# Kernel optimization log

Measured on AMD Instinct MI355X. Metric: run time of the kernel, lower is better.

## Reference

```python
import jax, jax.numpy as jnp
import numpy as np

N_H = 2048
N_EXC = 1638  # Dale's law: first N_EXC neurons excitatory, rest inhibitory
TAU_E, TAU_I = 0.02, 0.01
DT = 0.001
U_MIN_E, U_MAX_E = -5.0, 5.0
U_MIN_I, U_MAX_I = -5.0, 5.0
B, TR, T = 16, 4, 256


def setup_inputs() -> dict:
    key = jax.random.key(0)
    k1, k2, k3, k4, k5 = jax.random.split(key, 5)
    u0 = jax.random.normal(k1, (B, TR, N_H), dtype=jnp.float32)
    fs = jax.random.normal(k2, (B, TR, T, N_H), dtype=jnp.float32)
    # noise[..., 0, :] = eta0; noise[..., t, :] = eta used at step t; noise[..., T, :] = final eta
    noise = jax.random.normal(k3, (B, TR, T + 1, N_H), dtype=jnp.float32) * 0.1
    W_rec = jax.random.normal(k4, (N_H, N_H), dtype=jnp.float32) / np.sqrt(N_H)
    bias = jax.random.normal(k5, (N_H,), dtype=jnp.float32) * 0.01
    return {"u0": u0, "fs": fs, "noise": noise, "W_rec": W_rec, "bias": bias}


def _const_vectors():
    is_exc = jnp.arange(N_H) < N_EXC
    tau_inv = jnp.where(is_exc, 1.0 / TAU_E, 1.0 / TAU_I).astype(jnp.float32)  # diag(tau_inv) as vector
    u_max = jnp.where(is_exc, U_MAX_E, U_MAX_I).astype(jnp.float32)
    u_min = jnp.where(is_exc, U_MIN_E, U_MIN_I).astype(jnp.float32)
    return tau_inv, u_min, u_max


def reference(u0, fs, noise, W_rec, bias):
    tau_inv, u_min, u_max = _const_vectors()

    def step(u, inp):
        f, eta = inp  # each [B, TR, N_H]
        r = jax.nn.relu(u)  # rate_activation
        rec = jnp.einsum('btn,mn->btm', r, W_rec)  # W_rec(r), Linear-style r @ W^T
        du_dt = (-u + f + rec + bias + eta) * tau_inv  # @ diag(tau_inv)
        u_new = jnp.clip(u + du_dt * DT, u_min, u_max)
        return u_new, (u_new, du_dt)

    fs_t = jnp.moveaxis(fs, 2, 0)              # [T, B, TR, N_H]
    eta_t = jnp.moveaxis(noise[:, :, :T], 2, 0)  # [T, B, TR, N_H]
    _, (u_hist, du_hist) = jax.lax.scan(step, u0, (fs_t, eta_t))
    u_history = jnp.moveaxis(u_hist, 0, 2)     # [B, TR, T, N_H]
    du_dt_history = jnp.moveaxis(du_hist, 0, 2)
    eta_final = noise[:, :, T]
    return u_history, eta_final, du_dt_history
```

## Files before the change

### kernel.cpp

```cpp
#include <hip/hip_runtime.h>


#define N_H     2048
#define N_EXC   1638
#define T_STEPS 256
#define BT_TOT  64

typedef __bf16 bf16_t;
typedef __attribute__((ext_vector_type(8))) __bf16 bf16x8;
typedef __attribute__((ext_vector_type(4))) float  f32x4;
typedef __attribute__((ext_vector_type(2))) float  f32x2;

__global__ __launch_bounds__(256, 1)
void rnn_persistent(const float* __restrict__ u0,
                    const float* __restrict__ fs,
                    const float* __restrict__ noise,
                    const float* __restrict__ Wrec,
                    const float* __restrict__ bias,
                    float* __restrict__ out,
                    bf16_t* __restrict__ rbuf,
                    int* __restrict__ flags)
{
    const int g    = blockIdx.x;
    const int bti  = g >> 6;
    const int mi   = g & 63;
    const int tid  = threadIdx.x;
    const int wave = tid >> 6;
    const int lane = tid & 63;
    const int l15  = lane & 15;
    const int quad = lane >> 4;

    const int bt0 = bti * 16;
    const int m0  = mi * 32;
    const int kw0 = wave * 512;

    float* u_hist  = out;
    float* eta_out = out + (size_t)BT_TOT * T_STEPS * N_H;
    float* du_hist = eta_out + (size_t)BT_TOT * N_H;

    const int row  = tid >> 4;
    const int bt   = bt0 + row;
    const int nloc = (tid & 15) * 2;
    const int n0   = m0 + nloc;
    const int tile = nloc >> 4;
    const int col  = nloc & 15;
    const int srcl = (row >> 2) * 16 + col;
    const int reg  = row & 3;

    const f32x2 bv  = *(const f32x2*)(bias + n0);
    const float ti0 = (n0     < N_EXC) ? 50.0f : 100.0f;
    const float ti1 = (n0 + 1 < N_EXC) ? 50.0f : 100.0f;

    f32x2 uv = *(const f32x2*)(u0 + (size_t)bt * N_H + n0);
    float uA = uv.x, uB = uv.y;

    {
      union { bf16_t h[2]; unsigned int w; } rp;
      rp.h[0] = (bf16_t)fmaxf(uA, 0.0f);
      rp.h[1] = (bf16_t)fmaxf(uB, 0.0f);
      __hip_atomic_store((unsigned int*)(rbuf + (size_t)bt * N_H + n0), rp.w,
                         __ATOMIC_RELAXED, __HIP_MEMORY_SCOPE_AGENT);
    }
    asm volatile("s_waitcnt vmcnt(0)" ::: "memory");
    __syncthreads();
    if (tid == 0)
      __hip_atomic_store(&flags[g], 1, __ATOMIC_RELAXED, __HIP_MEMORY_SCOPE_AGENT);

    bf16x8 Wf[16][2];
#pragma unroll
    for (int kk = 0; kk < 16; ++kk) {
#pragma unroll
      for (int tl = 0; tl < 2; ++tl) {
        const float* wp = Wrec + (size_t)(m0 + tl*16 + l15) * N_H
                               + (kw0 + kk*32 + quad*8);
        f32x4 w0 = *(const f32x4*)(wp);
        f32x4 w1 = *(const f32x4*)(wp + 4);
        bf16x8 v;
#pragma unroll
        for (int j = 0; j < 4; ++j) { v[j] = (bf16_t)w0[j]; v[4+j] = (bf16_t)w1[j]; }
        Wf[kk][tl] = v;
      }
    }

    __shared__ float red[4][2][64][4];

    const size_t half = (size_t)BT_TOT * N_H;

    for (int t = 0; t < T_STEPS; ++t) {
      f32x2 fv = *(const f32x2*)(fs    + ((size_t)bt * T_STEPS       + t) * N_H + n0);
      f32x2 ev = *(const f32x2*)(noise + ((size_t)bt * (T_STEPS + 1) + t) * N_H + n0);

      if (wave == 0) {
        const int fi = (bti << 6) | lane;
        int cnt = 0;
        for (;;) {
          int v = __hip_atomic_load(&flags[fi], __ATOMIC_RELAXED,
                                    __HIP_MEMORY_SCOPE_AGENT);
          if (__all(v >= t + 1)) break;
          if (++cnt > (1 << 18)) break;
          __builtin_amdgcn_s_sleep(2);
        }
      }
      __syncthreads();

      const bf16_t* rsrc  = rbuf + (size_t)(t & 1) * half;
      const bf16_t* abase = rsrc + (size_t)(bt0 + l15) * N_H + (kw0 + quad * 8);
      bf16x8 af[16];
#define LOADA(I, OFFS) \
      asm volatile("global_load_dwordx4 %0, %1, off offset:" OFFS " sc0 sc1" \
                   : "=v"(af[I]) : "v"(abase) : "memory")
      LOADA(0,"0");    LOADA(1,"64");   LOADA(2,"128");  LOADA(3,"192");
      LOADA(4,"256");  LOADA(5,"320");  LOADA(6,"384");  LOADA(7,"448");
      LOADA(8,"512");  LOADA(9,"576");  LOADA(10,"640"); LOADA(11,"704");
      LOADA(12,"768"); LOADA(13,"832"); LOADA(14,"896"); LOADA(15,"960");
#undef LOADA
      asm volatile("s_waitcnt vmcnt(0)" ::: "memory");
      __builtin_amdgcn_sched_barrier(0);

      f32x4 acc0 = {0.f,0.f,0.f,0.f}, acc1 = {0.f,0.f,0.f,0.f};
#pragma unroll
      for (int kk = 0; kk < 16; ++kk) {
        acc0 = __builtin_amdgcn_mfma_f32_16x16x32_bf16(af[kk], Wf[kk][0], acc0, 0, 0, 0);
        acc1 = __builtin_amdgcn_mfma_f32_16x16x32_bf16(af[kk], Wf[kk][1], acc1, 0, 0, 0);
      }

      *reinterpret_cast<f32x4*>(&red[wave][0][lane][0]) = acc0;
      *reinterpret_cast<f32x4*>(&red[wave][1][lane][0]) = acc1;
      __syncthreads();

      float rec0 = red[0][tile][srcl][reg]     + red[1][tile][srcl][reg]
                 + red[2][tile][srcl][reg]     + red[3][tile][srcl][reg];
      float rec1 = red[0][tile][srcl + 1][reg] + red[1][tile][srcl + 1][reg]
                 + red[2][tile][srcl + 1][reg] + red[3][tile][srcl + 1][reg];

      float du0 = (-uA + fv.x + rec0 + bv.x + ev.x) * ti0;
      float du1 = (-uB + fv.y + rec1 + bv.y + ev.y) * ti1;
      float un0 = fminf(fmaxf(uA + du0 * 0.001f, -5.0f), 5.0f);
      float un1 = fminf(fmaxf(uB + du1 * 0.001f, -5.0f), 5.0f);
      uA = un0; uB = un1;

      {
        bf16_t* rdst = rbuf + (size_t)((t + 1) & 1) * half;
        union { bf16_t h[2]; unsigned int w; } rp;
        rp.h[0] = (bf16_t)fmaxf(un0, 0.0f);
        rp.h[1] = (bf16_t)fmaxf(un1, 0.0f);
        __hip_atomic_store((unsigned int*)(rdst + (size_t)bt * N_H + n0), rp.w,
                           __ATOMIC_RELAXED, __HIP_MEMORY_SCOPE_AGENT);
      }

      asm volatile("s_waitcnt vmcnt(0)" ::: "memory");
      __syncthreads();
      if (tid == 0)
        __hip_atomic_store(&flags[g], t + 2, __ATOMIC_RELAXED,
                           __HIP_MEMORY_SCOPE_AGENT);

      const size_t o = ((size_t)bt * T_STEPS + t) * N_H + n0;
      f32x2 uo; uo.x = un0; uo.y = un1;
      f32x2 dd; dd.x = du0; dd.y = du1;
      *(f32x2*)(u_hist + o)  = uo;
      *(f32x2*)(du_hist + o) = dd;
    }

    f32x2 ef = *(const f32x2*)(noise + ((size_t)bt * (T_STEPS + 1) + T_STEPS) * N_H + n0);
    *(f32x2*)(eta_out + (size_t)bt * N_H + n0) = ef;
}

extern "C" void kernel_launch(void* const* d_in, const int* in_sizes, int n_in,
                              void* d_out, int out_size, void* d_ws, size_t ws_size,
                              hipStream_t stream) {
    const float* u0    = (const float*)d_in[0];
    const float* fs    = (const float*)d_in[1];
    const float* noise = (const float*)d_in[2];
    const float* Wrec  = (const float*)d_in[3];
    const float* bias  = (const float*)d_in[4];
    float* out = (float*)d_out;

    int*    flags = (int*)d_ws;
    bf16_t* rbuf  = (bf16_t*)((char*)d_ws + 4096);

    hipMemsetAsync(d_ws, 0, 4096, stream);

    rnn_persistent<<<dim3(256), dim3(256), 0, stream>>>(
        u0, fs, noise, Wrec, bias, out, rbuf, flags);
}
```

Before: 1.789 ms.

## Use per-wave flags, drop block barriers, and pipeline MFMA with partial waitcnt

Replaces the per-block flag and block-wide barriers around the grid-wide step handshake with per-wave flags, so each wave signals and polls its own flags independently. All four waves now spin on the flags, burning FMAs instead of s_sleep. The reduction LDS buffer is double-buffered by step parity so the block barrier after the store can be removed. MFMA issue is split into four groups, each gated by a partial vmcnt wait so compute can overlap the remaining A-fragment loads. The risks are more polling traffic on the flags (four times as many, with four waves spinning) and subtle ordering issues from the removed barriers, and the flag array grows to 1024 ints.

Result: no change. 1.820 ms (+1.7%).

```diff
diff --git a/kernel.cpp b/kernel.cpp
--- a/kernel.cpp
+++ b/kernel.cpp
@@ -62,9 +62,9 @@
                          __ATOMIC_RELAXED, __HIP_MEMORY_SCOPE_AGENT);
     }
     asm volatile("s_waitcnt vmcnt(0)" ::: "memory");
-    __syncthreads();
-    if (tid == 0)
-      __hip_atomic_store(&flags[g], 1, __ATOMIC_RELAXED, __HIP_MEMORY_SCOPE_AGENT);
+    if (lane == 0)
+      __hip_atomic_store(&flags[(g << 2) | wave], 1,
+                         __ATOMIC_RELAXED, __HIP_MEMORY_SCOPE_AGENT);
 
     bf16x8 Wf[16][2];
 #pragma unroll
@@ -82,26 +82,31 @@
       }
     }
 
-    __shared__ float red[4][2][64][4];
+    __shared__ float red[2][4][2][65][4];
 
     const size_t half = (size_t)BT_TOT * N_H;
+    const int fi = (bti << 8) | (wave << 6) | lane;
 
     for (int t = 0; t < T_STEPS; ++t) {
       f32x2 fv = *(const f32x2*)(fs    + ((size_t)bt * T_STEPS       + t) * N_H + n0);
       f32x2 ev = *(const f32x2*)(noise + ((size_t)bt * (T_STEPS + 1) + t) * N_H + n0);
 
-      if (wave == 0) {
-        const int fi = (bti << 6) | lane;
+      {
+        float z0 = 1.0f + (float)lane * 1e-7f, z1 = 2.0f;
         int cnt = 0;
         for (;;) {
           int v = __hip_atomic_load(&flags[fi], __ATOMIC_RELAXED,
                                     __HIP_MEMORY_SCOPE_AGENT);
           if (__all(v >= t + 1)) break;
-          if (++cnt > (1 << 18)) break;
-          __builtin_amdgcn_s_sleep(2);
+          if (++cnt > (1 << 17)) break;
+#pragma unroll
+          for (int s = 0; s < 8; ++s) {
+            z0 = __builtin_fmaf(z0, 1.0000001f, 1e-20f);
+            z1 = __builtin_fmaf(z1, 0.9999999f, 1e-20f);
+          }
         }
+        asm volatile("" :: "v"(z0), "v"(z1));
       }
-      __syncthreads();
 
       const bf16_t* rsrc  = rbuf + (size_t)(t & 1) * half;
       const bf16_t* abase = rsrc + (size_t)(bt0 + l15) * N_H + (kw0 + quad * 8);
@@ -114,24 +119,34 @@
       LOADA(8,"512");  LOADA(9,"576");  LOADA(10,"640"); LOADA(11,"704");
       LOADA(12,"768"); LOADA(13,"832"); LOADA(14,"896"); LOADA(15,"960");
 #undef LOADA
-      asm volatile("s_waitcnt vmcnt(0)" ::: "memory");
-      __builtin_amdgcn_sched_barrier(0);
 
       f32x4 acc0 = {0.f,0.f,0.f,0.f}, acc1 = {0.f,0.f,0.f,0.f};
-#pragma unroll
-      for (int kk = 0; kk < 16; ++kk) {
-        acc0 = __builtin_amdgcn_mfma_f32_16x16x32_bf16(af[kk], Wf[kk][0], acc0, 0, 0, 0);
-        acc1 = __builtin_amdgcn_mfma_f32_16x16x32_bf16(af[kk], Wf[kk][1], acc1, 0, 0, 0);
-      }
+#define GRP(CNT, K0, K1, K2, K3) \
+      asm volatile("s_waitcnt vmcnt(" CNT ")" ::: "memory"); \
+      __builtin_amdgcn_sched_barrier(0); \
+      acc0 = __builtin_amdgcn_mfma_f32_16x16x32_bf16(af[K0], Wf[K0][0], acc0,0,0,0); \
+      acc1 = __builtin_amdgcn_mfma_f32_16x16x32_bf16(af[K0], Wf[K0][1], acc1,0,0,0); \
+      acc0 = __builtin_amdgcn_mfma_f32_16x16x32_bf16(af[K1], Wf[K1][0], acc0,0,0,0); \
+      acc1 = __builtin_amdgcn_mfma_f32_16x16x32_bf16(af[K1], Wf[K1][1], acc1,0,0,0); \
+      acc0 = __builtin_amdgcn_mfma_f32_16x16x32_bf16(af[K2], Wf[K2][0], acc0,0,0,0); \
+      acc1 = __builtin_amdgcn_mfma_f32_16x16x32_bf16(af[K2], Wf[K2][1], acc1,0,0,0); \
+      acc0 = __builtin_amdgcn_mfma_f32_16x16x32_bf16(af[K3], Wf[K3][0], acc0,0,0,0); \
+      acc1 = __builtin_amdgcn_mfma_f32_16x16x32_bf16(af[K3], Wf[K3][1], acc1,0,0,0)
+      GRP("12", 0, 1, 2, 3);
+      GRP("8",  4, 5, 6, 7);
+      GRP("4",  8, 9,10,11);
+      GRP("0", 12,13,14,15);
+#undef GRP
 
-      *reinterpret_cast<f32x4*>(&red[wave][0][lane][0]) = acc0;
-      *reinterpret_cast<f32x4*>(&red[wave][1][lane][0]) = acc1;
+      const int b = t & 1;
+      *reinterpret_cast<f32x4*>(&red[b][wave][0][lane][0]) = acc0;
+      *reinterpret_cast<f32x4*>(&red[b][wave][1][lane][0]) = acc1;
       __syncthreads();
 
-      float rec0 = red[0][tile][srcl][reg]     + red[1][tile][srcl][reg]
-                 + red[2][tile][srcl][reg]     + red[3][tile][srcl][reg];
-      float rec1 = red[0][tile][srcl + 1][reg] + red[1][tile][srcl + 1][reg]
-                 + red[2][tile][srcl + 1][reg] + red[3][tile][srcl + 1][reg];
+      float rec0 = red[b][0][tile][srcl][reg]     + red[b][1][tile][srcl][reg]
+                 + red[b][2][tile][srcl][reg]     + red[b][3][tile][srcl][reg];
+      float rec1 = red[b][0][tile][srcl + 1][reg] + red[b][1][tile][srcl + 1][reg]
+                 + red[b][2][tile][srcl + 1][reg] + red[b][3][tile][srcl + 1][reg];
 
       float du0 = (-uA + fv.x + rec0 + bv.x + ev.x) * ti0;
       float du1 = (-uB + fv.y + rec1 + bv.y + ev.y) * ti1;
@@ -149,10 +164,9 @@
       }
 
       asm volatile("s_waitcnt vmcnt(0)" ::: "memory");
-      __syncthreads();
-      if (tid == 0)
-        __hip_atomic_store(&flags[g], t + 2, __ATOMIC_RELAXED,
-                           __HIP_MEMORY_SCOPE_AGENT);
+      if (lane == 0)
+        __hip_atomic_store(&flags[(g << 2) | wave], t + 2,
+                           __ATOMIC_RELAXED, __HIP_MEMORY_SCOPE_AGENT);
 
       const size_t o = ((size_t)bt * T_STEPS + t) * N_H + n0;
       f32x2 uo; uo.x = un0; uo.y = un1;
```
